# Kernel optimization log

Measured on AMD Instinct MI355X. Metric: run time of the kernel, lower is better.

The kernel has to match this reference:

```python
import jax, jax.numpy as jnp
import numpy as np

B = 1; H = 192; W = 192; DIM = 128; HEADS = 8
WS = 16                      # window_size
OWS = 24                     # overlap_win_size = int(16*0.5)+16
PAD = 4                      # (OWS-WS)//2
C2 = DIM // 2                # per-branch channels
H2 = HEADS // 2              # per-branch heads
HID = 256                    # mlp_ratio * dim
TBL = (WS + OWS - 1) ** 2    # 1521 rel-pos table entries
SCALE = (C2 // H2) ** (-0.5) # head_dim ** -0.5


def layer_norm(x, w, b, eps=1e-5):
    mu = jnp.mean(x, -1, keepdims=True)
    var = jnp.mean((x - mu) ** 2, -1, keepdims=True)
    return (x - mu) * jax.lax.rsqrt(var + eps) * w + b


def window_partition(x, ws):
    b, h, w, c = x.shape
    x = x.reshape(b, h // ws, ws, w // ws, ws, c).transpose(0, 1, 3, 2, 4, 5)
    return x.reshape(-1, ws, ws, c)


def window_reverse(win, ws, h, w):
    b = win.shape[0] // ((h // ws) * (w // ws))
    x = win.reshape(b, h // ws, w // ws, ws, ws, -1).transpose(0, 1, 3, 2, 4, 5)
    return x.reshape(b, h, w, -1)


def _patch_idx(h, w):
    ri = (jnp.arange(h // WS) * WS)[:, None] + jnp.arange(OWS)  # (nwh, OWS)
    ci = (jnp.arange(w // WS) * WS)[:, None] + jnp.arange(OWS)  # (nww, OWS)
    return ri, ci


def unfold_patches(x):
    # x: (b, h, w, c) -> (b*nw, OWS*OWS, c); matches nn.Unfold(OWS, stride=WS, pad=PAD)
    b, h, w, c = x.shape
    xp = jnp.pad(x, ((0, 0), (PAD, PAD), (PAD, PAD), (0, 0)))
    ri, ci = _patch_idx(h, w)
    p = xp[:, ri[:, None, :, None], ci[None, :, None, :], :]  # (b,nwh,nww,OWS,OWS,c)
    return p.reshape(-1, OWS * OWS, c)


def fold_patches(p, b, h, w):
    # inverse of unfold: scatter-add overlapping patches into (b, h+2PAD, w+2PAD, c)
    nwh, nww = h // WS, w // WS
    c = p.shape[-1]
    p = p.reshape(b, nwh, nww, OWS, OWS, c)
    ri, ci = _patch_idx(h, w)
    canvas = jnp.zeros((b, h + 2 * PAD, w + 2 * PAD, c), p.dtype)
    return canvas.at[:, ri[:, None, :, None], ci[None, :, None, :], :].add(p)


def cubic_kernel(x, A=-0.75):
    # PyTorch bicubic (cubic convolution, A=-0.75)
    ax = jnp.abs(x)
    w1 = ((A + 2.0) * ax - (A + 3.0)) * ax * ax + 1.0
    w2 = A * (ax * (ax * (ax - 5.0) + 8.0) - 4.0)
    return jnp.where(ax <= 1.0, w1, jnp.where(ax < 2.0, w2, 0.0))


def resize_matrix(n_out, n_in):
    # dense 1-D bicubic resize matrix, align_corners=False, border-clamped (torch semantics)
    i = jnp.arange(n_out, dtype=jnp.float32)
    src = (i + 0.5) * (float(n_in) / float(n_out)) - 0.5
    fl = jnp.floor(src)
    idx = fl[:, None] + jnp.arange(-1, 3, dtype=jnp.float32)[None, :]  # (n_out, 4)
    wts = cubic_kernel(src[:, None] - idx)
    idx_c = jnp.clip(idx, 0, n_in - 1).astype(jnp.int32)
    M = jnp.zeros((n_out, n_in), jnp.float32)
    return M.at[jnp.arange(n_out)[:, None], idx_c].add(wts)


def cross_attn(xq, xkv, rpi, wq, wkv, rpb):
    b_, nq, d = xq.shape
    n = xkv.shape[1]
    q = (xq @ wq).reshape(b_, nq, H2, -1).transpose(0, 2, 1, 3)
    k, v = jnp.split(xkv @ wkv, 2, axis=-1)
    k = k.reshape(b_, n, H2, -1).transpose(0, 2, 1, 3)
    v = v.reshape(b_, n, H2, -1).transpose(0, 2, 1, 3)
    attn = jnp.einsum('bhqd,bhkd->bhqk', q * SCALE, k)
    bias = rpb[rpi.reshape(-1)].reshape(WS * WS, OWS * OWS, H2)
    bias = bias.transpose(2, 0, 1) if nq < n else bias.transpose(2, 1, 0)
    attn = jax.nn.softmax(attn + bias[None], axis=-1)
    out = jnp.einsum('bhqk,bhkd->bhqd', attn, v)
    return out.transpose(0, 2, 1, 3).reshape(b_, nq, d)


def gsfn(x, h, w, fc1_w, fc1_b, sgn_w, sgn_b, conv_w, conv_b, fc2_w, fc2_b):
    x = x @ fc1_w + fc1_b  # NOTE: source GSFN never applies self.act
    x1, x2 = jnp.split(x, 2, axis=-1)
    Bn, N, Ch = x2.shape
    x2 = layer_norm(x2, sgn_w, sgn_b).transpose(0, 2, 1).reshape(Bn, Ch, h, w)
    x2 = jax.lax.conv_general_dilated(
        x2, conv_w, (1, 1), ((1, 1), (1, 1)),
        feature_group_count=Ch, dimension_numbers=('NCHW', 'OIHW', 'NCHW'))
    x2 = x2 + conv_b[None, :, None, None]
    x2 = x2.reshape(Bn, Ch, N).transpose(0, 2, 1)
    return (x1 * x2) @ fc2_w + fc2_b


def mstb(x_tkn, ln1_w, ln1_b, q1_w, kv1_w, rpb1, q2_w, kv2_w, rpb2,
         proj_w, proj_b, ln2_w, ln2_b, fc1_w, fc1_b, sgn_w, sgn_b,
         conv_w, conv_b, fc2_w, fc2_b, rpi, h, w):
    b, _, c = x_tkn.shape
    short = x_tkn
    x = layer_norm(x_tkn, ln1_w, ln1_b).reshape(b, h, w, c)
    xw = window_partition(x, WS).reshape(-1, WS * WS, c)     # (b*nw, ws*ws, c)
    xa, xb = jnp.split(xw, 2, axis=-1)
    xb_img = window_reverse(xb.reshape(-1, WS, WS, C2), WS, h, w)  # (b,h,w,C2)
    xb_p = unfold_patches(xb_img)                            # (b*nw, OWS*OWS, C2)
    a = cross_attn(xa, xb_p, rpi, q1_w, kv1_w, rpb1) + xa
    bb = cross_attn(xb_p, xa, rpi, q2_w, kv2_w, rpb2) + xb_p
    folded = fold_patches(bb, b, h, w)                       # (b, h+2p, w+2p, C2)
    Mh = resize_matrix(h, h + 2 * PAD)
    Mw = resize_matrix(w, w + 2 * PAD)
    resized = jnp.einsum('oi,bijc,pj->bopc', Mh, folded, Mw)  # bicubic to (h,w)
    xb2 = window_partition(resized, WS).reshape(-1, WS * WS, C2)
    x = jnp.concatenate([a, xb2], -1)
    x = window_reverse(x.reshape(-1, WS, WS, c), WS, h, w).reshape(b, h * w, c)
    x = x @ proj_w + proj_b + short
    x = gsfn(layer_norm(x, ln2_w, ln2_b), h, w, fc1_w, fc1_b,
             sgn_w, sgn_b, conv_w, conv_b, fc2_w, fc2_b) + x
    return x


def setup_inputs() -> dict:
    key = jax.random.key(0)
    ks = jax.random.split(key, 12)
    rn = lambda k, s, sc: jax.random.normal(k, s, jnp.float32) * sc
    return {
        'x_tkn': jax.random.normal(ks[0], (B, H * W, DIM), jnp.float32),
        'ln1_w': jnp.ones((DIM,), jnp.float32), 'ln1_b': jnp.zeros((DIM,), jnp.float32),
        'q1_w': rn(ks[1], (C2, C2), 0.05), 'kv1_w': rn(ks[2], (C2, 2 * C2), 0.05),
        'rpb1': rn(ks[3], (TBL, H2), 0.02),
        'q2_w': rn(ks[4], (C2, C2), 0.05), 'kv2_w': rn(ks[5], (C2, 2 * C2), 0.05),
        'rpb2': rn(ks[6], (TBL, H2), 0.02),
        'proj_w': rn(ks[7], (DIM, DIM), 0.05), 'proj_b': jnp.zeros((DIM,), jnp.float32),
        'ln2_w': jnp.ones((DIM,), jnp.float32), 'ln2_b': jnp.zeros((DIM,), jnp.float32),
        'fc1_w': rn(ks[8], (DIM, HID), 0.05), 'fc1_b': jnp.zeros((HID,), jnp.float32),
        'sgn_w': jnp.ones((HID // 2,), jnp.float32), 'sgn_b': jnp.zeros((HID // 2,), jnp.float32),
        'conv_w': rn(ks[9], (HID // 2, 1, 3, 3), 0.1), 'conv_b': jnp.zeros((HID // 2,), jnp.float32),
        'fc2_w': rn(ks[10], (HID // 2, DIM), 0.05), 'fc2_b': jnp.zeros((DIM,), jnp.float32),
        'rpi': jax.random.randint(ks[11], (WS * WS, OWS * OWS), 0, TBL),
        'h': H, 'w': W,
    }


def reference(x_tkn, ln1_w, ln1_b, q1_w, kv1_w, rpb1, q2_w, kv2_w, rpb2,
              proj_w, proj_b, ln2_w, ln2_b, fc1_w, fc1_b, sgn_w, sgn_b,
              conv_w, conv_b, fc2_w, fc2_b, rpi, h, w):
    return mstb(x_tkn, ln1_w, ln1_b, q1_w, kv1_w, rpb1, q2_w, kv2_w, rpb2,
                proj_w, proj_b, ln2_w, ln2_b, fc1_w, fc1_b, sgn_w, sgn_b,
                conv_w, conv_b, fc2_w, fc2_b, rpi, h, w)
```

## Files before the change

### kernel.cpp

```cpp
#include <hip/hip_runtime.h>
#include <hip/hip_bf16.h>

#define HH 192
#define WW 192
#define NWIN 12
#define WSZ 16
#define OWSZ 24
#define PADK 4
#define NQ1 256
#define NKV1 576
#define C2K 64
#define H2K 4
#define HD 16
#define NTOK (HH*WW)
#define LOG2E 1.4426950408889634f
#define QSCALE (0.25f * LOG2E)

typedef __hip_bfloat16 bf16;
typedef __attribute__((ext_vector_type(8))) short bf16x8;
typedef __attribute__((ext_vector_type(4))) float f32x4;

union B8 { short s[8]; bf16x8 v; unsigned u[4]; };

__device__ __forceinline__ unsigned cvtpk(float lo, float hi)
{
    unsigned r;
    asm("v_cvt_pk_bf16_f32 %0, %1, %2" : "=v"(r) : "v"(lo), "v"(hi));
    return r;
}

__launch_bounds__(256)
__global__ void ln_kernel(const float* __restrict__ in, int is, int io,
                          float* __restrict__ out, int os, int oo,
                          const float* __restrict__ g, const float* __restrict__ b,
                          int M)
{
    int row = blockIdx.x * 4 + (threadIdx.x >> 6);
    if (row >= M) return;
    int lane = threadIdx.x & 63;
    const float* p = in + (size_t)row * is + io;
    float v0 = p[lane * 2], v1 = p[lane * 2 + 1];
    float s = v0 + v1, sq = v0 * v0 + v1 * v1;
#pragma unroll
    for (int o = 32; o > 0; o >>= 1) { s += __shfl_xor(s, o); sq += __shfl_xor(sq, o); }
    float mu  = s * 0.0078125f;
    float var = fmaxf(sq * 0.0078125f - mu * mu, 0.f);
    float inv = 1.0f / sqrtf(var + 1e-5f);
    float* q = out + (size_t)row * os + oo;
    q[lane * 2]     = (v0 - mu) * inv * g[lane * 2]     + b[lane * 2];
    q[lane * 2 + 1] = (v1 - mu) * inv * g[lane * 2 + 1] + b[lane * 2 + 1];
}

__global__ void wcombT_kernel(const float* __restrict__ q1_w, const float* __restrict__ kv1_w,
                              const float* __restrict__ q2_w, const float* __restrict__ kv2_w,
                              bf16* __restrict__ WT)
{
    int idx = blockIdx.x * 256 + threadIdx.x;
    if (idx >= 384 * 128) return;
    int c = idx >> 7, r = idx & 127;
    float v = 0.f;
    if (c < 64)       { if (r < 64)  v = q1_w[r * 64 + c] * QSCALE; }
    else if (c < 192) { if (r >= 64) v = kv1_w[(r - 64) * 128 + (c - 64)]; }
    else if (c < 256) { if (r >= 64) v = q2_w[(r - 64) * 64 + (c - 192)] * QSCALE; }
    else              { if (r < 64)  v = kv2_w[r * 128 + (c - 256)]; }
    WT[idx] = __float2bfloat16(v);
}

__global__ void wtrans_kernel(const float* __restrict__ src, int N, bf16* __restrict__ dst)
{
    int idx = blockIdx.x * 256 + threadIdx.x;
    if (idx >= N * 128) return;
    int n = idx >> 7, k = idx & 127;
    dst[idx] = __float2bfloat16(src[(size_t)k * N + n]);
}

__global__ void bias1_kernel(const float* __restrict__ rpb1, const int* __restrict__ rpi,
                             float* __restrict__ biasT)
{
    int idx = blockIdx.x * 256 + threadIdx.x;
    if (idx >= H2K * NKV1 * NQ1) return;
    int q = idx & 255;
    int n = (idx >> 8) % NKV1;
    int h = idx / (NKV1 * NQ1);
    biasT[idx] = rpb1[rpi[q * NKV1 + n] * H2K + h] * LOG2E;
}

__global__ void bias2_kernel(const float* __restrict__ rpb2, const int* __restrict__ rpi,
                             float* __restrict__ biasT)
{
    int idx = blockIdx.x * 256 + threadIdx.x;
    if (idx >= H2K * NQ1 * NKV1) return;
    int q = idx % NKV1;
    int k = (idx / NKV1) % NQ1;
    int h = idx / (NKV1 * NQ1);
    biasT[idx] = rpb2[rpi[k * NKV1 + q] * H2K + h] * LOG2E;
}

template<int NTPW, bool OBF>
__launch_bounds__(256)
__global__ void gemm_mfma(const float* __restrict__ A1, int a1s,
                          const float* __restrict__ A2, int a2s,
                          const bf16* __restrict__ WT,
                          const float* __restrict__ bias,
                          const float* __restrict__ R, int rs,
                          float* __restrict__ C, int cs)
{
    const int tid = threadIdx.x;
    const int lane = tid & 63, w = tid >> 6;
    const int g = lane >> 4, nl = lane & 15;

    bf16x8 wf[NTPW][4];
#pragma unroll
    for (int t = 0; t < NTPW; t++) {
        const bf16* wp = WT + (size_t)((w * NTPW + t) * 16 + nl) * 128;
#pragma unroll
        for (int ks = 0; ks < 4; ks++)
            wf[t][ks] = *(const bf16x8*)(wp + ks * 32 + 8 * g);
    }

    const f32x4 zz = {0.f, 0.f, 0.f, 0.f};
    const int row = (blockIdx.x * 4 + blockIdx.y) * 16 + nl;

    bf16x8 xf[4];
    const float* ap = A1 + (size_t)row * a1s + 8 * g;
#pragma unroll
    for (int ks = 0; ks < 4; ks++) {
        float4 v0 = *(const float4*)(ap + ks * 32);
        float4 v1 = *(const float4*)(ap + ks * 32 + 4);
        if (A2) {
            const float* ap2 = A2 + (size_t)row * a2s + 8 * g + ks * 32;
            float4 m0 = *(const float4*)(ap2);
            float4 m1 = *(const float4*)(ap2 + 4);
            v0.x *= m0.x; v0.y *= m0.y; v0.z *= m0.z; v0.w *= m0.w;
            v1.x *= m1.x; v1.y *= m1.y; v1.z *= m1.z; v1.w *= m1.w;
        }
        B8 f;
        f.u[0] = cvtpk(v0.x, v0.y);
        f.u[1] = cvtpk(v0.z, v0.w);
        f.u[2] = cvtpk(v1.x, v1.y);
        f.u[3] = cvtpk(v1.z, v1.w);
        xf[ks] = f.v;
    }

    f32x4 acc[NTPW];
#pragma unroll
    for (int t = 0; t < NTPW; t++) acc[t] = zz;
#pragma unroll
    for (int ks = 0; ks < 4; ks++)
#pragma unroll
        for (int t = 0; t < NTPW; t++)
            acc[t] = __builtin_amdgcn_mfma_f32_16x16x32_bf16(wf[t][ks], xf[ks], acc[t], 0, 0, 0);

#pragma unroll
    for (int t = 0; t < NTPW; t++) {
        const int n0t = (w * NTPW + t) * 16 + 4 * g;
        if (OBF) {
            unsigned* Cu = (unsigned*)C + (size_t)row * (cs >> 1) + (n0t >> 1);
            uint2 o;
            o.x = cvtpk(acc[t][0], acc[t][1]);
            o.y = cvtpk(acc[t][2], acc[t][3]);
            *(uint2*)Cu = o;
        } else {
            float4 o;
            o.x = acc[t][0]; o.y = acc[t][1]; o.z = acc[t][2]; o.w = acc[t][3];
            if (bias) {
                float4 bv = *(const float4*)(bias + n0t);
                o.x += bv.x; o.y += bv.y; o.z += bv.z; o.w += bv.w;
            }
            if (R) {
                float4 rv = *(const float4*)(R + (size_t)row * rs + n0t);
                o.x += rv.x; o.y += rv.y; o.z += rv.z; o.w += rv.w;
            }
            *(float4*)(C + (size_t)row * cs + n0t) = o;
        }
    }
}

__launch_bounds__(256)
__global__ void attn1_mfma(const unsigned* __restrict__ qkvu,
                           const float* __restrict__ lnx,
                           const float* __restrict__ biasT,
                           float* __restrict__ xcat)
{
    __shared__ unsigned K_lds[NKV1][10];
    __shared__ unsigned V_lds[NKV1][10];

    const int win = blockIdx.x, h = blockIdx.y;
    const int wi = win / NWIN, wj = win % NWIN;
    const int tid = threadIdx.x;
    const int lane = tid & 63, w = tid >> 6;
    const int g = lane >> 4, qloc = lane & 15;

    for (int n = tid; n < NKV1; n += 256) {
        int rr = wi * WSZ - PADK + n / OWSZ, cc = wj * WSZ - PADK + n % OWSZ;
        bool ib = (rr >= 0 && rr < HH && cc >= 0 && cc < WW);
        uint4 k0v = make_uint4(0, 0, 0, 0), k1v = k0v, v0v = k0v, v1v = k0v;
        if (ib) {
            const unsigned* src = qkvu + (size_t)(rr * WW + cc) * 96 + 32 + 8 * h;
            k0v = *(const uint4*)(src);
            k1v = *(const uint4*)(src + 4);
            v0v = *(const uint4*)(src + 32);
            v1v = *(const uint4*)(src + 36);
        }
        *(uint4*)&K_lds[n][0] = k0v; *(uint4*)&K_lds[n][4] = k1v;
        *(uint4*)&V_lds[n][0] = v0v; *(uint4*)&V_lds[n][4] = v1v;
    }
    __syncthreads();

    const int q0base = blockIdx.z * 128 + w * 32;
    bf16x8 qfrag[2];
#pragma unroll
    for (int qt = 0; qt < 2; qt++) {
        int q = q0base + qt * 16 + qloc;
        int pix = (wi * WSZ + (q >> 4)) * WW + wj * WSZ + (q & 15);
        B8 f;
#pragma unroll
        for (int j = 0; j < 4; j++) f.u[j] = 0;
        if (g < 2)
            f.v = *(const bf16x8*)(qkvu + (size_t)pix * 96 + 8 * h + 4 * g);
        qfrag[qt] = f.v;
    }

    f32x4 O[2];
    float lsum[2];
#pragma unroll
    for (int qt = 0; qt < 2; qt++) { O[qt] = (f32x4){0.f, 0.f, 0.f, 0.f}; lsum[qt] = 0.f; }
    const f32x4 zz = {0.f, 0.f, 0.f, 0.f};

    for (int step = 0; step < 18; step++) {
        const int k0 = step * 32;
        bf16x8 kfA, kfB;
        if (g < 2) {
            kfA = *(const bf16x8*)&K_lds[k0 + qloc][4 * g];
            kfB = *(const bf16x8*)&K_lds[k0 + 16 + qloc][4 * g];
        } else {
            B8 zf;
#pragma unroll
            for (int j = 0; j < 4; j++) zf.u[j] = 0;
            kfA = zf.v; kfB = zf.v;
        }
        B8 vf;
#pragma unroll
        for (int j = 0; j < 8; j++) {
            int key = k0 + 4 * g + (j & 3) + ((j >> 2) << 4);
            unsigned word = V_lds[key][qloc >> 1];
            vf.s[j] = (short)((qloc & 1) ? (word >> 16) : (word & 0xffff));
        }

#pragma unroll
        for (int qt = 0; qt < 2; qt++) {
            f32x4 sA = __builtin_amdgcn_mfma_f32_16x16x32_bf16(kfA, qfrag[qt], zz, 0, 0, 0);
            f32x4 sB = __builtin_amdgcn_mfma_f32_16x16x32_bf16(kfB, qfrag[qt], zz, 0, 0, 0);
            int qa = q0base + qt * 16 + qloc;
            const float* bpA = biasT + ((size_t)h * NKV1 + k0 + 4 * g) * NQ1 + qa;
            const float* bpB = bpA + 16 * NQ1;
            float pa[4], pb[4];
            float ls = 0.f;
#pragma unroll
            for (int r = 0; r < 4; r++) {
                pa[r] = exp2f(sA[r] + bpA[(size_t)r * NQ1]);
                pb[r] = exp2f(sB[r] + bpB[(size_t)r * NQ1]);
                ls += pa[r] + pb[r];
            }
            B8 pf;
            pf.u[0] = cvtpk(pa[0], pa[1]);
            pf.u[1] = cvtpk(pa[2], pa[3]);
            pf.u[2] = cvtpk(pb[0], pb[1]);
            pf.u[3] = cvtpk(pb[2], pb[3]);
            lsum[qt] += ls;
            O[qt] = __builtin_amdgcn_mfma_f32_16x16x32_bf16(vf.v, pf.v, O[qt], 0, 0, 0);
        }
    }

#pragma unroll
    for (int qt = 0; qt < 2; qt++) {
        float lt = lsum[qt];
        lt += __shfl_xor(lt, 16);
        lt += __shfl_xor(lt, 32);
        float rl = 1.f / lt;
        int q = q0base + qt * 16 + qloc;
        int pix = (wi * WSZ + (q >> 4)) * WW + wj * WSZ + (q & 15);
        size_t base = (size_t)pix * 128 + h * HD + 4 * g;
#pragma unroll
        for (int r = 0; r < 4; r++)
            xcat[base + r] = O[qt][r] * rl + lnx[base + r];
    }
}

__launch_bounds__(256)
__global__ void attn2_mfma(const unsigned* __restrict__ qkvu,
                           const float* __restrict__ lnx,
                           const float* __restrict__ biasT,
                           float* __restrict__ bb)
{
    __shared__ unsigned K_lds[NQ1][10];
    __shared__ unsigned V_lds[NQ1][10];

    const int win = blockIdx.x, h = blockIdx.y;
    const int wi = win / NWIN, wj = win % NWIN;
    const int tid = threadIdx.x;
    const int lane = tid & 63, w = tid >> 6;
    const int g = lane >> 4, qloc = lane & 15;

    {
        int n = tid;
        int pix = (wi * WSZ + (n >> 4)) * WW + wj * WSZ + (n & 15);
        const unsigned* src = qkvu + (size_t)pix * 96 + 32 + 8 * h;
        *(uint4*)&K_lds[n][0] = *(const uint4*)(src);
        *(uint4*)&K_lds[n][4] = *(const uint4*)(src + 4);
        *(uint4*)&V_lds[n][0] = *(const uint4*)(src + 32);
        *(uint4*)&V_lds[n][4] = *(const uint4*)(src + 36);
    }
    __syncthreads();

    const int q0base = blockIdx.z * 192 + w * 48;
    bf16x8 qfrag[3];
    bool qin[3];
    int qpix[3];
#pragma unroll
    for (int qt = 0; qt < 3; qt++) {
        int qa = q0base + qt * 16 + qloc;
        int gr = wi * WSZ - PADK + qa / OWSZ, gc = wj * WSZ - PADK + qa % OWSZ;
        bool ib = (gr >= 0 && gr < HH && gc >= 0 && gc < WW);
        qin[qt] = ib;
        qpix[qt] = ib ? gr * WW + gc : 0;
        B8 f;
#pragma unroll
        for (int j = 0; j < 4; j++) f.u[j] = 0;
        if (ib && g < 2)
            f.v = *(const bf16x8*)(qkvu + (size_t)qpix[qt] * 96 + 8 * h + 4 * g);
        qfrag[qt] = f.v;
    }

    f32x4 O[3];
    float lsum[3];
#pragma unroll
    for (int qt = 0; qt < 3; qt++) { O[qt] = (f32x4){0.f, 0.f, 0.f, 0.f}; lsum[qt] = 0.f; }
    const f32x4 zz = {0.f, 0.f, 0.f, 0.f};

    for (int step = 0; step < 8; step++) {
        const int k0 = step * 32;
        bf16x8 kfA, kfB;
        if (g < 2) {
            kfA = *(const bf16x8*)&K_lds[k0 + qloc][4 * g];
            kfB = *(const bf16x8*)&K_lds[k0 + 16 + qloc][4 * g];
        } else {
            B8 zf;
#pragma unroll
            for (int j = 0; j < 4; j++) zf.u[j] = 0;
            kfA = zf.v; kfB = zf.v;
        }
        B8 vf;
#pragma unroll
        for (int j = 0; j < 8; j++) {
            int key = k0 + 4 * g + (j & 3) + ((j >> 2) << 4);
            unsigned word = V_lds[key][qloc >> 1];
            vf.s[j] = (short)((qloc & 1) ? (word >> 16) : (word & 0xffff));
        }

#pragma unroll
        for (int qt = 0; qt < 3; qt++) {
            f32x4 sA = __builtin_amdgcn_mfma_f32_16x16x32_bf16(kfA, qfrag[qt], zz, 0, 0, 0);
            f32x4 sB = __builtin_amdgcn_mfma_f32_16x16x32_bf16(kfB, qfrag[qt], zz, 0, 0, 0);
            int qa = q0base + qt * 16 + qloc;
            const float* bpA = biasT + ((size_t)h * NQ1 + k0 + 4 * g) * NKV1 + qa;
            const float* bpB = bpA + 16 * NKV1;
            float pa[4], pb[4];
            float ls = 0.f;
#pragma unroll
            for (int r = 0; r < 4; r++) {
                pa[r] = exp2f(sA[r] + bpA[(size_t)r * NKV1]);
                pb[r] = exp2f(sB[r] + bpB[(size_t)r * NKV1]);
                ls += pa[r] + pb[r];
            }
            B8 pf;
            pf.u[0] = cvtpk(pa[0], pa[1]);
            pf.u[1] = cvtpk(pa[2], pa[3]);
            pf.u[2] = cvtpk(pb[0], pb[1]);
            pf.u[3] = cvtpk(pb[2], pb[3]);
            lsum[qt] += ls;
            O[qt] = __builtin_amdgcn_mfma_f32_16x16x32_bf16(vf.v, pf.v, O[qt], 0, 0, 0);
        }
    }

#pragma unroll
    for (int qt = 0; qt < 3; qt++) {
        float lt = lsum[qt];
        lt += __shfl_xor(lt, 16);
        lt += __shfl_xor(lt, 32);
        float rl = 1.f / lt;
        int qa = q0base + qt * 16 + qloc;
        size_t obase = ((size_t)win * NKV1 + qa) * C2K + h * HD + 4 * g;
        size_t rbase = (size_t)qpix[qt] * 128 + C2K + h * HD + 4 * g;
#pragma unroll
        for (int r = 0; r < 4; r++)
            bb[obase + r] = O[qt][r] * rl + (qin[qt] ? lnx[rbase + r] : 0.f);
    }
}

__global__ void fold_kernel(const float* __restrict__ bb, float* __restrict__ folded)
{
    int idx = blockIdx.x * 256 + threadIdx.x;
    if (idx >= 200 * 200 * 64) return;
    int c = idx & 63;
    int j = (idx >> 6) % 200;
    int i = idx / (64 * 200);
    int ilo = (i > 23) ? ((i - 8) >> 4) : 0;
    int ihi = min(11, i >> 4);
    int jlo = (j > 23) ? ((j - 8) >> 4) : 0;
    int jhi = min(11, j >> 4);
    float s = 0.f;
    for (int wi = ilo; wi <= ihi; wi++)
        for (int wj = jlo; wj <= jhi; wj++) {
            int p = (i - wi * 16) * OWSZ + (j - wj * 16);
            s += bb[((size_t)(wi * NWIN + wj) * NKV1 + p) * C2K + c];
        }
    folded[idx] = s;
}

__device__ __forceinline__ float cubicw(float x)
{
    float ax = fabsf(x);
    const float A = -0.75f;
    if (ax <= 1.f) return ((A + 2.f) * ax - (A + 3.f)) * ax * ax + 1.f;
    if (ax < 2.f)  return A * (ax * (ax * (ax - 5.f) + 8.f) - 4.f);
    return 0.f;
}

__global__ void resize_kernel(const float* __restrict__ folded, float* __restrict__ xcat)
{
    int idx = blockIdx.x * 256 + threadIdx.x;
    if (idx >= HH * WW * C2K) return;
    int c = idx & 63;
    int p = (idx >> 6) % WW;
    int o = idx / (C2K * WW);
    const float ratio = 200.f / 192.f;
    float sr = (o + 0.5f) * ratio - 0.5f;
    float sc = (p + 0.5f) * ratio - 0.5f;
    int fr = (int)floorf(sr), fcc = (int)floorf(sc);
    float wc[4]; int ic[4];
#pragma unroll
    for (int u = 0; u < 4; u++) {
        int jj = fcc - 1 + u;
        wc[u] = cubicw(sc - (float)jj);
        ic[u] = min(max(jj, 0), 199);
    }
    float acc = 0.f;
#pragma unroll
    for (int t = 0; t < 4; t++) {
        int ii = fr - 1 + t;
        float wr = cubicw(sr - (float)ii);
        int ir = min(max(ii, 0), 199);
        const float* rowp = folded + ((size_t)ir * 200) * 64 + c;
        float rs = 0.f;
#pragma unroll
        for (int u = 0; u < 4; u++) rs += wc[u] * rowp[(size_t)ic[u] * 64];
        acc += wr * rs;
    }
    xcat[(size_t)(o * WW + p) * 128 + C2K + c] = acc;
}

__launch_bounds__(256)
__global__ void proj_ln2(const float* __restrict__ A1,
                         const bf16* __restrict__ WT,
                         const float* __restrict__ bias,
                         const float* __restrict__ R,
                         const float* __restrict__ ln2w, const float* __restrict__ ln2b,
                         float* __restrict__ xbuf, unsigned* __restrict__ ybf)
{
    __shared__ float psum[16][16];
    __shared__ float psq[16][16];
    __shared__ float mu_s[16], inv_s[16];

    const int tid = threadIdx.x;
    const int lane = tid & 63, w = tid >> 6;
    const int g = lane >> 4, nl = lane & 15;

    bf16x8 wf[2][4];
#pragma unroll
    for (int t = 0; t < 2; t++) {
        const bf16* wp = WT + (size_t)((w * 2 + t) * 16 + nl) * 128;
#pragma unroll
        for (int ks = 0; ks < 4; ks++)
            wf[t][ks] = *(const bf16x8*)(wp + ks * 32 + 8 * g);
    }

    const int row = (blockIdx.x * 4 + blockIdx.y) * 16 + nl;
    bf16x8 xf[4];
    const float* ap = A1 + (size_t)row * 128 + 8 * g;
#pragma unroll
    for (int ks = 0; ks < 4; ks++) {
        float4 v0 = *(const float4*)(ap + ks * 32);
        float4 v1 = *(const float4*)(ap + ks * 32 + 4);
        B8 f;
        f.u[0] = cvtpk(v0.x, v0.y);
        f.u[1] = cvtpk(v0.z, v0.w);
        f.u[2] = cvtpk(v1.x, v1.y);
        f.u[3] = cvtpk(v1.z, v1.w);
        xf[ks] = f.v;
    }

    const f32x4 zz = {0.f, 0.f, 0.f, 0.f};
    f32x4 acc[2];
    acc[0] = zz; acc[1] = zz;
#pragma unroll
    for (int ks = 0; ks < 4; ks++) {
        acc[0] = __builtin_amdgcn_mfma_f32_16x16x32_bf16(wf[0][ks], xf[ks], acc[0], 0, 0, 0);
        acc[1] = __builtin_amdgcn_mfma_f32_16x16x32_bf16(wf[1][ks], xf[ks], acc[1], 0, 0, 0);
    }

    float o[2][4];
    float s = 0.f, sq = 0.f;
#pragma unroll
    for (int t = 0; t < 2; t++) {
        int n0t = (w * 2 + t) * 16 + 4 * g;
        float4 bv = *(const float4*)(bias + n0t);
        float4 rv = *(const float4*)(R + (size_t)row * 128 + n0t);
        o[t][0] = acc[t][0] + bv.x + rv.x;
        o[t][1] = acc[t][1] + bv.y + rv.y;
        o[t][2] = acc[t][2] + bv.z + rv.z;
        o[t][3] = acc[t][3] + bv.w + rv.w;
#pragma unroll
        for (int r = 0; r < 4; r++) { s += o[t][r]; sq += o[t][r] * o[t][r]; }
    }
    psum[nl][w * 4 + g] = s;
    psq[nl][w * 4 + g] = sq;
    __syncthreads();
    if (tid < 16) {
        float ts = 0.f, tq = 0.f;
#pragma unroll
        for (int i = 0; i < 16; i++) { ts += psum[tid][i]; tq += psq[tid][i]; }
        float mu = ts * 0.0078125f;
        float var = fmaxf(tq * 0.0078125f - mu * mu, 0.f);
        mu_s[tid] = mu;
        inv_s[tid] = 1.0f / sqrtf(var + 1e-5f);
    }
    __syncthreads();

    float mu = mu_s[nl], inv = inv_s[nl];
#pragma unroll
    for (int t = 0; t < 2; t++) {
        int n0t = (w * 2 + t) * 16 + 4 * g;
        *(float4*)(xbuf + (size_t)row * 128 + n0t) = make_float4(o[t][0], o[t][1], o[t][2], o[t][3]);
        float4 gw = *(const float4*)(ln2w + n0t);
        float4 gb = *(const float4*)(ln2b + n0t);
        float y0 = (o[t][0] - mu) * inv * gw.x + gb.x;
        float y1 = (o[t][1] - mu) * inv * gw.y + gb.y;
        float y2 = (o[t][2] - mu) * inv * gw.z + gb.z;
        float y3 = (o[t][3] - mu) * inv * gw.w + gb.w;
        uint2 yo;
        yo.x = cvtpk(y0, y1);
        yo.y = cvtpk(y2, y3);
        *(uint2*)(ybf + (size_t)row * 64 + (n0t >> 1)) = yo;
    }
}

__launch_bounds__(256)
__global__ void fc1_sgn(const unsigned* __restrict__ ybf,
                        const bf16* __restrict__ WT,
                        const float* __restrict__ bias,
                        const float* __restrict__ sgnw, const float* __restrict__ sgnb,
                        float* __restrict__ h1)
{
    __shared__ float psum[16][8];
    __shared__ float psq[16][8];
    __shared__ float mu_s[16], inv_s[16];

    const int tid = threadIdx.x;
    const int lane = tid & 63, w = tid >> 6;
    const int g = lane >> 4, nl = lane & 15;

    bf16x8 wf[4][4];
#pragma unroll
    for (int t = 0; t < 4; t++) {
        const bf16* wp = WT + (size_t)((w * 4 + t) * 16 + nl) * 128;
#pragma unroll
        for (int ks = 0; ks < 4; ks++)
            wf[t][ks] = *(const bf16x8*)(wp + ks * 32 + 8 * g);
    }

    const int row = (blockIdx.x * 4 + blockIdx.y) * 16 + nl;
    bf16x8 xf[4];
    const unsigned* ap = ybf + (size_t)row * 64 + 4 * g;
#pragma unroll
    for (int ks = 0; ks < 4; ks++)
        xf[ks] = *(const bf16x8*)(ap + ks * 16);

    const f32x4 zz = {0.f, 0.f, 0.f, 0.f};
    f32x4 acc[4];
#pragma unroll
    for (int t = 0; t < 4; t++) acc[t] = zz;
#pragma unroll
    for (int ks = 0; ks < 4; ks++)
#pragma unroll
        for (int t = 0; t < 4; t++)
            acc[t] = __builtin_amdgcn_mfma_f32_16x16x32_bf16(wf[t][ks], xf[ks], acc[t], 0, 0, 0);

    float o[4][4];
    float s = 0.f, sq = 0.f;
#pragma unroll
    for (int t = 0; t < 4; t++) {
        int n0t = (w * 4 + t) * 16 + 4 * g;
        float4 bv = *(const float4*)(bias + n0t);
        o[t][0] = acc[t][0] + bv.x;
        o[t][1] = acc[t][1] + bv.y;
        o[t][2] = acc[t][2] + bv.z;
        o[t][3] = acc[t][3] + bv.w;
    }
    if (w >= 2) {
#pragma unroll
        for (int t = 0; t < 4; t++)
#pragma unroll
            for (int r = 0; r < 4; r++) { s += o[t][r]; sq += o[t][r] * o[t][r]; }
        psum[nl][(w - 2) * 4 + g] = s;
        psq[nl][(w - 2) * 4 + g] = sq;
    }
    __syncthreads();
    if (tid < 16) {
        float ts = 0.f, tq = 0.f;
#pragma unroll
        for (int i = 0; i < 8; i++) { ts += psum[tid][i]; tq += psq[tid][i]; }
        float mu = ts * 0.0078125f;
        float var = fmaxf(tq * 0.0078125f - mu * mu, 0.f);
        mu_s[tid] = mu;
        inv_s[tid] = 1.0f / sqrtf(var + 1e-5f);
    }
    __syncthreads();

    if (w < 2) {
#pragma unroll
        for (int t = 0; t < 4; t++) {
            int n0t = (w * 4 + t) * 16 + 4 * g;
            *(float4*)(h1 + (size_t)row * 256 + n0t) = make_float4(o[t][0], o[t][1], o[t][2], o[t][3]);
        }
    } else {
        float mu = mu_s[nl], inv = inv_s[nl];
#pragma unroll
        for (int t = 0; t < 4; t++) {
            int n0t = (w * 4 + t) * 16 + 4 * g;
            float4 gw = *(const float4*)(sgnw + n0t - 128);
            float4 gb = *(const float4*)(sgnb + n0t - 128);
            float4 y;
            y.x = (o[t][0] - mu) * inv * gw.x + gb.x;
            y.y = (o[t][1] - mu) * inv * gw.y + gb.y;
            y.z = (o[t][2] - mu) * inv * gw.z + gb.z;
            y.w = (o[t][3] - mu) * inv * gw.w + gb.w;
            *(float4*)(h1 + (size_t)row * 256 + n0t) = y;
        }
    }
}

__global__ void dwconv_kernel(const float* __restrict__ x2n,
                              const float* __restrict__ conv_w,
                              const float* __restrict__ conv_b,
                              float* __restrict__ x2c)
{
    int idx = blockIdx.x * 256 + threadIdx.x;
    if (idx >= NTOK * 128) return;
    int ch = idx & 127, t = idx >> 7;
    int i = t / WW, j = t % WW;
    float acc = conv_b[ch];
#pragma unroll
    for (int a = 0; a < 3; a++) {
        int ii = i + a - 1;
        if (ii < 0 || ii >= HH) continue;
#pragma unroll
        for (int b = 0; b < 3; b++) {
            int jj = j + b - 1;
            if (jj < 0 || jj >= WW) continue;
            acc += conv_w[ch * 9 + a * 3 + b] * x2n[(size_t)(ii * WW + jj) * 256 + ch];
        }
    }
    x2c[(size_t)t * 128 + ch] = acc;
}

extern "C" void kernel_launch(void* const* d_in, const int* in_sizes, int n_in,
                              void* d_out, int out_size, void* d_ws, size_t ws_size,
                              hipStream_t stream)
{
    (void)in_sizes; (void)n_in; (void)out_size; (void)ws_size;
    const float* x_tkn  = (const float*)d_in[0];
    const float* ln1_w  = (const float*)d_in[1];
    const float* ln1_b  = (const float*)d_in[2];
    const float* q1_w   = (const float*)d_in[3];
    const float* kv1_w  = (const float*)d_in[4];
    const float* rpb1   = (const float*)d_in[5];
    const float* q2_w   = (const float*)d_in[6];
    const float* kv2_w  = (const float*)d_in[7];
    const float* rpb2   = (const float*)d_in[8];
    const float* proj_w = (const float*)d_in[9];
    const float* proj_b = (const float*)d_in[10];
    const float* ln2_w  = (const float*)d_in[11];
    const float* ln2_b  = (const float*)d_in[12];
    const float* fc1_w  = (const float*)d_in[13];
    const float* fc1_b  = (const float*)d_in[14];
    const float* sgn_w  = (const float*)d_in[15];
    const float* sgn_b  = (const float*)d_in[16];
    const float* conv_w = (const float*)d_in[17];
    const float* conv_b = (const float*)d_in[18];
    const float* fc2_w  = (const float*)d_in[19];
    const float* fc2_b  = (const float*)d_in[20];
    const int*   rpi    = (const int*)d_in[21];

    float* ws = (float*)d_ws;
    float* lnx    = ws;
    float* xcat   = ws + 4718592;
    float* bbuf   = ws + 9437184;
    bf16*  projT  = (bf16*)(ws + 14155776);
    bf16*  fc1T   = (bf16*)(ws + 14163968);
    bf16*  fc2T   = (bf16*)(ws + 14180352);
    float* bias1T = ws + 14745600;
    float* bias2T = ws + 17104896;
    float* qkv    = ws + 17694720;
    bf16*  wcombT = (bf16*)(ws + 21233664);
    float* foldp  = ws + 17694720;
    float* h1     = ws + 14745600;
    float* out    = (float*)d_out;
    unsigned* ybf = (unsigned*)bbuf;

    ln_kernel<<<NTOK / 4, 256, 0, stream>>>(x_tkn, 128, 0, lnx, 128, 0, ln1_w, ln1_b, NTOK);
    wcombT_kernel<<<(384 * 128) / 256, 256, 0, stream>>>(q1_w, kv1_w, q2_w, kv2_w, wcombT);
    bias1_kernel<<<(H2K * NKV1 * NQ1) / 256, 256, 0, stream>>>(rpb1, rpi, bias1T);
    bias2_kernel<<<(H2K * NQ1 * NKV1) / 256, 256, 0, stream>>>(rpb2, rpi, bias2T);
    gemm_mfma<3, true><<<dim3(NTOK / 64, 4), 256, 0, stream>>>(lnx, 128, nullptr, 0, wcombT,
                                                               nullptr, nullptr, 0, qkv, 192);
    attn1_mfma<<<dim3(144, 4, 2), 256, 0, stream>>>((const unsigned*)qkv, lnx, bias1T, xcat);
    gemm_mfma<3, true><<<dim3(NTOK / 64, 4), 256, 0, stream>>>(lnx, 128, nullptr, 0,
                                                               wcombT + 192 * 128,
                                                               nullptr, nullptr, 0, qkv, 192);
    attn2_mfma<<<dim3(144, 4, 3), 256, 0, stream>>>((const unsigned*)qkv, lnx, bias2T, bbuf);
    fold_kernel<<<(200 * 200 * 64) / 256, 256, 0, stream>>>(bbuf, foldp);
    wtrans_kernel<<<(128 * 128) / 256, 256, 0, stream>>>(proj_w, 128, projT);
    wtrans_kernel<<<(256 * 128) / 256, 256, 0, stream>>>(fc1_w, 256, fc1T);
    wtrans_kernel<<<(128 * 128) / 256, 256, 0, stream>>>(fc2_w, 128, fc2T);
    resize_kernel<<<(HH * WW * C2K) / 256, 256, 0, stream>>>(foldp, xcat);
    proj_ln2<<<dim3(NTOK / 64, 4), 256, 0, stream>>>(xcat, projT, proj_b, x_tkn,
                                                     ln2_w, ln2_b, lnx, ybf);
    fc1_sgn<<<dim3(NTOK / 64, 4), 256, 0, stream>>>(ybf, fc1T, fc1_b, sgn_w, sgn_b, h1);
    dwconv_kernel<<<(NTOK * 128) / 256, 256, 0, stream>>>(h1 + 128, conv_w, conv_b, xcat);
    gemm_mfma<2, false><<<dim3(NTOK / 64, 4), 256, 0, stream>>>(h1, 256, xcat, 128, fc2T,
                                                                fc2_b, lnx, 128, out, 128);
}
```

Baseline: 305.1 us.

## Fuse LN1 into QKV GEMM, merge attention branches, bf16 MLP intermediates

LayerNorm1 is folded into a single QKV GEMM that computes all 384 output columns in one pass and also writes lnx. The two attention kernels become one launch that selects the branch from blockIdx, so both branches can run concurrently. The fc1/SGN outputs and the dwconv gating product are stored as bf16, with the gate multiply moved into dwconv, to cut memory traffic. The final GEMM then reads bf16 A directly, at some cost in intermediate precision.

After: 285.9 us. -6.3%, faster.

```diff
diff --git a/kernel.cpp b/kernel.cpp
--- a/kernel.cpp
+++ b/kernel.cpp
@@ -28,27 +28,9 @@
     asm("v_cvt_pk_bf16_f32 %0, %1, %2" : "=v"(r) : "v"(lo), "v"(hi));
     return r;
 }
-
-__launch_bounds__(256)
-__global__ void ln_kernel(const float* __restrict__ in, int is, int io,
-                          float* __restrict__ out, int os, int oo,
-                          const float* __restrict__ g, const float* __restrict__ b,
-                          int M)
-{
-    int row = blockIdx.x * 4 + (threadIdx.x >> 6);
-    if (row >= M) return;
-    int lane = threadIdx.x & 63;
-    const float* p = in + (size_t)row * is + io;
-    float v0 = p[lane * 2], v1 = p[lane * 2 + 1];
-    float s = v0 + v1, sq = v0 * v0 + v1 * v1;
-#pragma unroll
-    for (int o = 32; o > 0; o >>= 1) { s += __shfl_xor(s, o); sq += __shfl_xor(sq, o); }
-    float mu  = s * 0.0078125f;
-    float var = fmaxf(sq * 0.0078125f - mu * mu, 0.f);
-    float inv = 1.0f / sqrtf(var + 1e-5f);
-    float* q = out + (size_t)row * os + oo;
-    q[lane * 2]     = (v0 - mu) * inv * g[lane * 2]     + b[lane * 2];
-    q[lane * 2 + 1] = (v1 - mu) * inv * g[lane * 2 + 1] + b[lane * 2 + 1];
+__device__ __forceinline__ float bfu2f(unsigned short u)
+{
+    return __uint_as_float(((unsigned)u) << 16);
 }
 
 __global__ void wcombT_kernel(const float* __restrict__ q1_w, const float* __restrict__ kv1_w,
@@ -96,305 +78,307 @@
     biasT[idx] = rpb2[rpi[k * NKV1 + q] * H2K + h] * LOG2E;
 }
 
-template<int NTPW, bool OBF>
 __launch_bounds__(256)
-__global__ void gemm_mfma(const float* __restrict__ A1, int a1s,
-                          const float* __restrict__ A2, int a2s,
-                          const bf16* __restrict__ WT,
-                          const float* __restrict__ bias,
-                          const float* __restrict__ R, int rs,
-                          float* __restrict__ C, int cs)
+__global__ void gemm_qkv(const float* __restrict__ x_tkn,
+                         const float* __restrict__ ln1w, const float* __restrict__ ln1b,
+                         const bf16* __restrict__ WT,
+                         unsigned* __restrict__ qkvo, float* __restrict__ lnx)
 {
     const int tid = threadIdx.x;
     const int lane = tid & 63, w = tid >> 6;
     const int g = lane >> 4, nl = lane & 15;
 
-    bf16x8 wf[NTPW][4];
-#pragma unroll
-    for (int t = 0; t < NTPW; t++) {
-        const bf16* wp = WT + (size_t)((w * NTPW + t) * 16 + nl) * 128;
+    bf16x8 wf[6][4];
+#pragma unroll
+    for (int t = 0; t < 6; t++) {
+        const bf16* wp = WT + (size_t)((w * 6 + t) * 16 + nl) * 128;
 #pragma unroll
         for (int ks = 0; ks < 4; ks++)
             wf[t][ks] = *(const bf16x8*)(wp + ks * 32 + 8 * g);
     }
 
-    const f32x4 zz = {0.f, 0.f, 0.f, 0.f};
     const int row = (blockIdx.x * 4 + blockIdx.y) * 16 + nl;
-
-    bf16x8 xf[4];
-    const float* ap = A1 + (size_t)row * a1s + 8 * g;
+    const float* ap = x_tkn + (size_t)row * 128 + 8 * g;
+
+    float av[4][8];
+    float s = 0.f, sq = 0.f;
 #pragma unroll
     for (int ks = 0; ks < 4; ks++) {
         float4 v0 = *(const float4*)(ap + ks * 32);
         float4 v1 = *(const float4*)(ap + ks * 32 + 4);
-        if (A2) {
-            const float* ap2 = A2 + (size_t)row * a2s + 8 * g + ks * 32;
-            float4 m0 = *(const float4*)(ap2);
-            float4 m1 = *(const float4*)(ap2 + 4);
-            v0.x *= m0.x; v0.y *= m0.y; v0.z *= m0.z; v0.w *= m0.w;
-            v1.x *= m1.x; v1.y *= m1.y; v1.z *= m1.z; v1.w *= m1.w;
+        av[ks][0] = v0.x; av[ks][1] = v0.y; av[ks][2] = v0.z; av[ks][3] = v0.w;
+        av[ks][4] = v1.x; av[ks][5] = v1.y; av[ks][6] = v1.z; av[ks][7] = v1.w;
+#pragma unroll
+        for (int j = 0; j < 8; j++) { s += av[ks][j]; sq += av[ks][j] * av[ks][j]; }
+    }
+    s  += __shfl_xor(s, 16);  s  += __shfl_xor(s, 32);
+    sq += __shfl_xor(sq, 16); sq += __shfl_xor(sq, 32);
+    float mu  = s * 0.0078125f;
+    float var = fmaxf(sq * 0.0078125f - mu * mu, 0.f);
+    float inv = 1.0f / sqrtf(var + 1e-5f);
+
+    bf16x8 xf[4];
+#pragma unroll
+    for (int ks = 0; ks < 4; ks++) {
+        int col = ks * 32 + 8 * g;
+        float4 g0 = *(const float4*)(ln1w + col);
+        float4 g1 = *(const float4*)(ln1w + col + 4);
+        float4 b0 = *(const float4*)(ln1b + col);
+        float4 b1 = *(const float4*)(ln1b + col + 4);
+        float nv[8];
+        nv[0] = (av[ks][0] - mu) * inv * g0.x + b0.x;
+        nv[1] = (av[ks][1] - mu) * inv * g0.y + b0.y;
+        nv[2] = (av[ks][2] - mu) * inv * g0.z + b0.z;
+        nv[3] = (av[ks][3] - mu) * inv * g0.w + b0.w;
+        nv[4] = (av[ks][4] - mu) * inv * g1.x + b1.x;
+        nv[5] = (av[ks][5] - mu) * inv * g1.y + b1.y;
+        nv[6] = (av[ks][6] - mu) * inv * g1.z + b1.z;
+        nv[7] = (av[ks][7] - mu) * inv * g1.w + b1.w;
+        if (w == 0) {
+            float* lp = lnx + (size_t)row * 128 + col;
+            *(float4*)lp       = make_float4(nv[0], nv[1], nv[2], nv[3]);
+            *(float4*)(lp + 4) = make_float4(nv[4], nv[5], nv[6], nv[7]);
         }
         B8 f;
-        f.u[0] = cvtpk(v0.x, v0.y);
-        f.u[1] = cvtpk(v0.z, v0.w);
-        f.u[2] = cvtpk(v1.x, v1.y);
-        f.u[3] = cvtpk(v1.z, v1.w);
+        f.u[0] = cvtpk(nv[0], nv[1]);
+        f.u[1] = cvtpk(nv[2], nv[3]);
+        f.u[2] = cvtpk(nv[4], nv[5]);
+        f.u[3] = cvtpk(nv[6], nv[7]);
         xf[ks] = f.v;
     }
 
-    f32x4 acc[NTPW];
-#pragma unroll
-    for (int t = 0; t < NTPW; t++) acc[t] = zz;
+    const f32x4 zz = {0.f, 0.f, 0.f, 0.f};
+    f32x4 acc[6];
+#pragma unroll
+    for (int t = 0; t < 6; t++) acc[t] = zz;
 #pragma unroll
     for (int ks = 0; ks < 4; ks++)
 #pragma unroll
-        for (int t = 0; t < NTPW; t++)
+        for (int t = 0; t < 6; t++)
             acc[t] = __builtin_amdgcn_mfma_f32_16x16x32_bf16(wf[t][ks], xf[ks], acc[t], 0, 0, 0);
 
 #pragma unroll
-    for (int t = 0; t < NTPW; t++) {
-        const int n0t = (w * NTPW + t) * 16 + 4 * g;
-        if (OBF) {
-            unsigned* Cu = (unsigned*)C + (size_t)row * (cs >> 1) + (n0t >> 1);
-            uint2 o;
-            o.x = cvtpk(acc[t][0], acc[t][1]);
-            o.y = cvtpk(acc[t][2], acc[t][3]);
-            *(uint2*)Cu = o;
-        } else {
-            float4 o;
-            o.x = acc[t][0]; o.y = acc[t][1]; o.z = acc[t][2]; o.w = acc[t][3];
-            if (bias) {
-                float4 bv = *(const float4*)(bias + n0t);
-                o.x += bv.x; o.y += bv.y; o.z += bv.z; o.w += bv.w;
-            }
-            if (R) {
-                float4 rv = *(const float4*)(R + (size_t)row * rs + n0t);
-                o.x += rv.x; o.y += rv.y; o.z += rv.z; o.w += rv.w;
-            }
-            *(float4*)(C + (size_t)row * cs + n0t) = o;
-        }
+    for (int t = 0; t < 6; t++) {
+        int n0t = (w * 6 + t) * 16 + 4 * g;
+        uint2 o;
+        o.x = cvtpk(acc[t][0], acc[t][1]);
+        o.y = cvtpk(acc[t][2], acc[t][3]);
+        *(uint2*)(qkvo + (size_t)row * 192 + (n0t >> 1)) = o;
     }
 }
 
 __launch_bounds__(256)
-__global__ void attn1_mfma(const unsigned* __restrict__ qkvu,
+__global__ void attn_fused(const unsigned* __restrict__ qkvu,
                            const float* __restrict__ lnx,
-                           const float* __restrict__ biasT,
-                           float* __restrict__ xcat)
+                           const float* __restrict__ bias1T,
+                           const float* __restrict__ bias2T,
+                           float* __restrict__ xcat,
+                           float* __restrict__ bb)
 {
     __shared__ unsigned K_lds[NKV1][10];
     __shared__ unsigned V_lds[NKV1][10];
 
-    const int win = blockIdx.x, h = blockIdx.y;
-    const int wi = win / NWIN, wj = win % NWIN;
+    const int h = blockIdx.y;
     const int tid = threadIdx.x;
     const int lane = tid & 63, w = tid >> 6;
     const int g = lane >> 4, qloc = lane & 15;
-
-    for (int n = tid; n < NKV1; n += 256) {
-        int rr = wi * WSZ - PADK + n / OWSZ, cc = wj * WSZ - PADK + n % OWSZ;
-        bool ib = (rr >= 0 && rr < HH && cc >= 0 && cc < WW);
-        uint4 k0v = make_uint4(0, 0, 0, 0), k1v = k0v, v0v = k0v, v1v = k0v;
-        if (ib) {
-            const unsigned* src = qkvu + (size_t)(rr * WW + cc) * 96 + 32 + 8 * h;
-            k0v = *(const uint4*)(src);
-            k1v = *(const uint4*)(src + 4);
-            v0v = *(const uint4*)(src + 32);
-            v1v = *(const uint4*)(src + 36);
-        }
-        *(uint4*)&K_lds[n][0] = k0v; *(uint4*)&K_lds[n][4] = k1v;
-        *(uint4*)&V_lds[n][0] = v0v; *(uint4*)&V_lds[n][4] = v1v;
-    }
-    __syncthreads();
-
-    const int q0base = blockIdx.z * 128 + w * 32;
-    bf16x8 qfrag[2];
-#pragma unroll
-    for (int qt = 0; qt < 2; qt++) {
-        int q = q0base + qt * 16 + qloc;
-        int pix = (wi * WSZ + (q >> 4)) * WW + wj * WSZ + (q & 15);
-        B8 f;
-#pragma unroll
-        for (int j = 0; j < 4; j++) f.u[j] = 0;
-        if (g < 2)
-            f.v = *(const bf16x8*)(qkvu + (size_t)pix * 96 + 8 * h + 4 * g);
-        qfrag[qt] = f.v;
-    }
-
-    f32x4 O[2];
-    float lsum[2];
-#pragma unroll
-    for (int qt = 0; qt < 2; qt++) { O[qt] = (f32x4){0.f, 0.f, 0.f, 0.f}; lsum[qt] = 0.f; }
     const f32x4 zz = {0.f, 0.f, 0.f, 0.f};
 
-    for (int step = 0; step < 18; step++) {
-        const int k0 = step * 32;
-        bf16x8 kfA, kfB;
-        if (g < 2) {
-            kfA = *(const bf16x8*)&K_lds[k0 + qloc][4 * g];
-            kfB = *(const bf16x8*)&K_lds[k0 + 16 + qloc][4 * g];
-        } else {
-            B8 zf;
-#pragma unroll
-            for (int j = 0; j < 4; j++) zf.u[j] = 0;
-            kfA = zf.v; kfB = zf.v;
-        }
-        B8 vf;
-#pragma unroll
-        for (int j = 0; j < 8; j++) {
-            int key = k0 + 4 * g + (j & 3) + ((j >> 2) << 4);
-            unsigned word = V_lds[key][qloc >> 1];
-            vf.s[j] = (short)((qloc & 1) ? (word >> 16) : (word & 0xffff));
-        }
-
+    if (blockIdx.x < 288) {
+        const int win = blockIdx.x % 144, z = blockIdx.x / 144;
+        const int wi = win / NWIN, wj = win % NWIN;
+
+        for (int n = tid; n < NKV1; n += 256) {
+            int rr = wi * WSZ - PADK + n / OWSZ, cc = wj * WSZ - PADK + n % OWSZ;
+            bool ib = (rr >= 0 && rr < HH && cc >= 0 && cc < WW);
+            uint4 k0v = make_uint4(0, 0, 0, 0), k1v = k0v, v0v = k0v, v1v = k0v;
+            if (ib) {
+                const unsigned* src = qkvu + (size_t)(rr * WW + cc) * 192 + 32 + 8 * h;
+                k0v = *(const uint4*)(src);
+                k1v = *(const uint4*)(src + 4);
+                v0v = *(const uint4*)(src + 32);
+                v1v = *(const uint4*)(src + 36);
+            }
+            *(uint4*)&K_lds[n][0] = k0v; *(uint4*)&K_lds[n][4] = k1v;
+            *(uint4*)&V_lds[n][0] = v0v; *(uint4*)&V_lds[n][4] = v1v;
+        }
+        __syncthreads();
+
+        const int q0base = z * 128 + w * 32;
+        bf16x8 qfrag[2];
 #pragma unroll
         for (int qt = 0; qt < 2; qt++) {
-            f32x4 sA = __builtin_amdgcn_mfma_f32_16x16x32_bf16(kfA, qfrag[qt], zz, 0, 0, 0);
-            f32x4 sB = __builtin_amdgcn_mfma_f32_16x16x32_bf16(kfB, qfrag[qt], zz, 0, 0, 0);
+            int q = q0base + qt * 16 + qloc;
+            int pix = (wi * WSZ + (q >> 4)) * WW + wj * WSZ + (q & 15);
+            B8 f;
+#pragma unroll
+            for (int j = 0; j < 4; j++) f.u[j] = 0;
+            if (g < 2)
+                f.v = *(const bf16x8*)(qkvu + (size_t)pix * 192 + 8 * h + 4 * g);
+            qfrag[qt] = f.v;
+        }
+
+        f32x4 O[2];
+        float lsum[2];
+#pragma unroll
+        for (int qt = 0; qt < 2; qt++) { O[qt] = zz; lsum[qt] = 0.f; }
+
+        for (int step = 0; step < 18; step++) {
+            const int k0 = step * 32;
+            bf16x8 kfA, kfB;
+            if (g < 2) {
+                kfA = *(const bf16x8*)&K_lds[k0 + qloc][4 * g];
+                kfB = *(const bf16x8*)&K_lds[k0 + 16 + qloc][4 * g];
+            } else {
+                B8 zf;
+#pragma unroll
+                for (int j = 0; j < 4; j++) zf.u[j] = 0;
+                kfA = zf.v; kfB = zf.v;
+            }
+            B8 vf;
+#pragma unroll
+            for (int j = 0; j < 8; j++) {
+                int key = k0 + 4 * g + (j & 3) + ((j >> 2) << 4);
+                unsigned word = V_lds[key][qloc >> 1];
+                vf.s[j] = (short)((qloc & 1) ? (word >> 16) : (word & 0xffff));
+            }
+
+#pragma unroll
+            for (int qt = 0; qt < 2; qt++) {
+                f32x4 sA = __builtin_amdgcn_mfma_f32_16x16x32_bf16(kfA, qfrag[qt], zz, 0, 0, 0);
+                f32x4 sB = __builtin_amdgcn_mfma_f32_16x16x32_bf16(kfB, qfrag[qt], zz, 0, 0, 0);
+                int qa = q0base + qt * 16 + qloc;
+                const float* bpA = bias1T + ((size_t)h * NKV1 + k0 + 4 * g) * NQ1 + qa;
+                const float* bpB = bpA + 16 * NQ1;
+                float pa[4], pb[4];
+                float ls = 0.f;
+#pragma unroll
+                for (int r = 0; r < 4; r++) {
+                    pa[r] = exp2f(sA[r] + bpA[(size_t)r * NQ1]);
+                    pb[r] = exp2f(sB[r] + bpB[(size_t)r * NQ1]);
+                    ls += pa[r] + pb[r];
+                }
+                B8 pf;
+                pf.u[0] = cvtpk(pa[0], pa[1]);
+                pf.u[1] = cvtpk(pa[2], pa[3]);
+                pf.u[2] = cvtpk(pb[0], pb[1]);
+                pf.u[3] = cvtpk(pb[2], pb[3]);
+                lsum[qt] += ls;
+                O[qt] = __builtin_amdgcn_mfma_f32_16x16x32_bf16(vf.v, pf.v, O[qt], 0, 0, 0);
+            }
+        }
+
+#pragma unroll
+        for (int qt = 0; qt < 2; qt++) {
+            float lt = lsum[qt];
+            lt += __shfl_xor(lt, 16);
+            lt += __shfl_xor(lt, 32);
+            float rl = 1.f / lt;
+            int q = q0base + qt * 16 + qloc;
+            int pix = (wi * WSZ + (q >> 4)) * WW + wj * WSZ + (q & 15);
+            size_t base = (size_t)pix * 128 + h * HD + 4 * g;
+#pragma unroll
+            for (int r = 0; r < 4; r++)
+                xcat[base + r] = O[qt][r] * rl + lnx[base + r];
+        }
+    } else {
+        const int bx = blockIdx.x - 288;
+        const int win = bx % 144, z = bx / 144;
+        const int wi = win / NWIN, wj = win % NWIN;
+
+        {
+            int n = tid;
+            int pix = (wi * WSZ + (n >> 4)) * WW + wj * WSZ + (n & 15);
+            const unsigned* src = qkvu + (size_t)pix * 192 + 128 + 8 * h;
+            *(uint4*)&K_lds[n][0] = *(const uint4*)(src);
+            *(uint4*)&K_lds[n][4] = *(const uint4*)(src + 4);
+            *(uint4*)&V_lds[n][0] = *(const uint4*)(src + 32);
+            *(uint4*)&V_lds[n][4] = *(const uint4*)(src + 36);
+        }
+        __syncthreads();
+
+        const int q0base = z * 192 + w * 48;
+        bf16x8 qfrag[3];
+        bool qin[3];
+        int qpix[3];
+#pragma unroll
+        for (int qt = 0; qt < 3; qt++) {
             int qa = q0base + qt * 16 + qloc;
-            const float* bpA = biasT + ((size_t)h * NKV1 + k0 + 4 * g) * NQ1 + qa;
-            const float* bpB = bpA + 16 * NQ1;
-            float pa[4], pb[4];
-            float ls = 0.f;
-#pragma unroll
-            for (int r = 0; r < 4; r++) {
-                pa[r] = exp2f(sA[r] + bpA[(size_t)r * NQ1]);
-                pb[r] = exp2f(sB[r] + bpB[(size_t)r * NQ1]);
-                ls += pa[r] + pb[r];
+            int gr = wi * WSZ - PADK + qa / OWSZ, gc = wj * WSZ - PADK + qa % OWSZ;
+            bool ib = (gr >= 0 && gr < HH && gc >= 0 && gc < WW);
+            qin[qt] = ib;
+            qpix[qt] = ib ? gr * WW + gc : 0;
+            B8 f;
+#pragma unroll
+            for (int j = 0; j < 4; j++) f.u[j] = 0;
+            if (ib && g < 2)
+                f.v = *(const bf16x8*)(qkvu + (size_t)qpix[qt] * 192 + 96 + 8 * h + 4 * g);
+            qfrag[qt] = f.v;
+        }
+
+        f32x4 O[3];
+        float lsum[3];
+#pragma unroll
+        for (int qt = 0; qt < 3; qt++) { O[qt] = zz; lsum[qt] = 0.f; }
+
+        for (int step = 0; step < 8; step++) {
+            const int k0 = step * 32;
+            bf16x8 kfA, kfB;
+            if (g < 2) {
+                kfA = *(const bf16x8*)&K_lds[k0 + qloc][4 * g];
+                kfB = *(const bf16x8*)&K_lds[k0 + 16 + qloc][4 * g];
+            } else {
+                B8 zf;
+#pragma unroll
+                for (int j = 0; j < 4; j++) zf.u[j] = 0;
+                kfA = zf.v; kfB = zf.v;
             }
-            B8 pf;
-            pf.u[0] = cvtpk(pa[0], pa[1]);
-            pf.u[1] = cvtpk(pa[2], pa[3]);
-            pf.u[2] = cvtpk(pb[0], pb[1]);
-            pf.u[3] = cvtpk(pb[2], pb[3]);
-            lsum[qt] += ls;
-            O[qt] = __builtin_amdgcn_mfma_f32_16x16x32_bf16(vf.v, pf.v, O[qt], 0, 0, 0);
-        }
-    }
-
-#pragma unroll
-    for (int qt = 0; qt < 2; qt++) {
-        float lt = lsum[qt];
-        lt += __shfl_xor(lt, 16);
-        lt += __shfl_xor(lt, 32);
-        float rl = 1.f / lt;
-        int q = q0base + qt * 16 + qloc;
-        int pix = (wi * WSZ + (q >> 4)) * WW + wj * WSZ + (q & 15);
-        size_t base = (size_t)pix * 128 + h * HD + 4 * g;
-#pragma unroll
-        for (int r = 0; r < 4; r++)
-            xcat[base + r] = O[qt][r] * rl + lnx[base + r];
-    }
-}
-
-__launch_bounds__(256)
-__global__ void attn2_mfma(const unsigned* __restrict__ qkvu,
-                           const float* __restrict__ lnx,
-                           const float* __restrict__ biasT,
-                           float* __restrict__ bb)
-{
-    __shared__ unsigned K_lds[NQ1][10];
-    __shared__ unsigned V_lds[NQ1][10];
-
-    const int win = blockIdx.x, h = blockIdx.y;
-    const int wi = win / NWIN, wj = win % NWIN;
-    const int tid = threadIdx.x;
-    const int lane = tid & 63, w = tid >> 6;
-    const int g = lane >> 4, qloc = lane & 15;
-
-    {
-        int n = tid;
-        int pix = (wi * WSZ + (n >> 4)) * WW + wj * WSZ + (n & 15);
-        const unsigned* src = qkvu + (size_t)pix * 96 + 32 + 8 * h;
-        *(uint4*)&K_lds[n][0] = *(const uint4*)(src);
-        *(uint4*)&K_lds[n][4] = *(const uint4*)(src + 4);
-        *(uint4*)&V_lds[n][0] = *(const uint4*)(src + 32);
-        *(uint4*)&V_lds[n][4] = *(const uint4*)(src + 36);
-    }
-    __syncthreads();
-
-    const int q0base = blockIdx.z * 192 + w * 48;
-    bf16x8 qfrag[3];
-    bool qin[3];
-    int qpix[3];
-#pragma unroll
-    for (int qt = 0; qt < 3; qt++) {
-        int qa = q0base + qt * 16 + qloc;
-        int gr = wi * WSZ - PADK + qa / OWSZ, gc = wj * WSZ - PADK + qa % OWSZ;
-        bool ib = (gr >= 0 && gr < HH && gc >= 0 && gc < WW);
-        qin[qt] = ib;
-        qpix[qt] = ib ? gr * WW + gc : 0;
-        B8 f;
-#pragma unroll
-        for (int j = 0; j < 4; j++) f.u[j] = 0;
-        if (ib && g < 2)
-            f.v = *(const bf16x8*)(qkvu + (size_t)qpix[qt] * 96 + 8 * h + 4 * g);
-        qfrag[qt] = f.v;
-    }
-
-    f32x4 O[3];
-    float lsum[3];
-#pragma unroll
-    for (int qt = 0; qt < 3; qt++) { O[qt] = (f32x4){0.f, 0.f, 0.f, 0.f}; lsum[qt] = 0.f; }
-    const f32x4 zz = {0.f, 0.f, 0.f, 0.f};
-
-    for (int step = 0; step < 8; step++) {
-        const int k0 = step * 32;
-        bf16x8 kfA, kfB;
-        if (g < 2) {
-            kfA = *(const bf16x8*)&K_lds[k0 + qloc][4 * g];
-            kfB = *(const bf16x8*)&K_lds[k0 + 16 + qloc][4 * g];
-        } else {
-            B8 zf;
-#pragma unroll
-            for (int j = 0; j < 4; j++) zf.u[j] = 0;
-            kfA = zf.v; kfB = zf.v;
-        }
-        B8 vf;
-#pragma unroll
-        for (int j = 0; j < 8; j++) {
-            int key = k0 + 4 * g + (j & 3) + ((j >> 2) << 4);
-            unsigned word = V_lds[key][qloc >> 1];
-            vf.s[j] = (short)((qloc & 1) ? (word >> 16) : (word & 0xffff));
+            B8 vf;
+#pragma unroll
+            for (int j = 0; j < 8; j++) {
+                int key = k0 + 4 * g + (j & 3) + ((j >> 2) << 4);
+                unsigned word = V_lds[key][qloc >> 1];
+                vf.s[j] = (short)((qloc & 1) ? (word >> 16) : (word & 0xffff));
+            }
+
+#pragma unroll
+            for (int qt = 0; qt < 3; qt++) {
+                f32x4 sA = __builtin_amdgcn_mfma_f32_16x16x32_bf16(kfA, qfrag[qt], zz, 0, 0, 0);
+                f32x4 sB = __builtin_amdgcn_mfma_f32_16x16x32_bf16(kfB, qfrag[qt], zz, 0, 0, 0);
+                int qa = q0base + qt * 16 + qloc;
+                const float* bpA = bias2T + ((size_t)h * NQ1 + k0 + 4 * g) * NKV1 + qa;
+                const float* bpB = bpA + 16 * NKV1;
+                float pa[4], pb[4];
+                float ls = 0.f;
+#pragma unroll
+                for (int r = 0; r < 4; r++) {
+                    pa[r] = exp2f(sA[r] + bpA[(size_t)r * NKV1]);
+                    pb[r] = exp2f(sB[r] + bpB[(size_t)r * NKV1]);
+                    ls += pa[r] + pb[r];
+                }
+                B8 pf;
+                pf.u[0] = cvtpk(pa[0], pa[1]);
+                pf.u[1] = cvtpk(pa[2], pa[3]);
+                pf.u[2] = cvtpk(pb[0], pb[1]);
+                pf.u[3] = cvtpk(pb[2], pb[3]);
+                lsum[qt] += ls;
+                O[qt] = __builtin_amdgcn_mfma_f32_16x16x32_bf16(vf.v, pf.v, O[qt], 0, 0, 0);
+            }
         }
 
 #pragma unroll
         for (int qt = 0; qt < 3; qt++) {
-            f32x4 sA = __builtin_amdgcn_mfma_f32_16x16x32_bf16(kfA, qfrag[qt], zz, 0, 0, 0);
-            f32x4 sB = __builtin_amdgcn_mfma_f32_16x16x32_bf16(kfB, qfrag[qt], zz, 0, 0, 0);
+            float lt = lsum[qt];
+            lt += __shfl_xor(lt, 16);
+            lt += __shfl_xor(lt, 32);
+            float rl = 1.f / lt;
             int qa = q0base + qt * 16 + qloc;
-            const float* bpA = biasT + ((size_t)h * NQ1 + k0 + 4 * g) * NKV1 + qa;
-            const float* bpB = bpA + 16 * NKV1;
-            float pa[4], pb[4];
-            float ls = 0.f;
-#pragma unroll
-            for (int r = 0; r < 4; r++) {
-                pa[r] = exp2f(sA[r] + bpA[(size_t)r * NKV1]);
-                pb[r] = exp2f(sB[r] + bpB[(size_t)r * NKV1]);
-                ls += pa[r] + pb[r];
-            }
-            B8 pf;
-            pf.u[0] = cvtpk(pa[0], pa[1]);
-            pf.u[1] = cvtpk(pa[2], pa[3]);
-            pf.u[2] = cvtpk(pb[0], pb[1]);
-            pf.u[3] = cvtpk(pb[2], pb[3]);
-            lsum[qt] += ls;
-            O[qt] = __builtin_amdgcn_mfma_f32_16x16x32_bf16(vf.v, pf.v, O[qt], 0, 0, 0);
-        }
-    }
-
-#pragma unroll
-    for (int qt = 0; qt < 3; qt++) {
-        float lt = lsum[qt];
-        lt += __shfl_xor(lt, 16);
-        lt += __shfl_xor(lt, 32);
-        float rl = 1.f / lt;
-        int qa = q0base + qt * 16 + qloc;
-        size_t obase = ((size_t)win * NKV1 + qa) * C2K + h * HD + 4 * g;
-        size_t rbase = (size_t)qpix[qt] * 128 + C2K + h * HD + 4 * g;
-#pragma unroll
-        for (int r = 0; r < 4; r++)
-            bb[obase + r] = O[qt][r] * rl + (qin[qt] ? lnx[rbase + r] : 0.f);
+            size_t obase = ((size_t)win * NKV1 + qa) * C2K + h * HD + 4 * g;
+            size_t rbase = (size_t)qpix[qt] * 128 + C2K + h * HD + 4 * g;
+#pragma unroll
+            for (int r = 0; r < 4; r++)
+                bb[obase + r] = O[qt][r] * rl + (qin[qt] ? lnx[rbase + r] : 0.f);
+        }
     }
 }
 
@@ -560,7 +544,7 @@
                         const bf16* __restrict__ WT,
                         const float* __restrict__ bias,
                         const float* __restrict__ sgnw, const float* __restrict__ sgnb,
-                        float* __restrict__ h1)
+                        unsigned* __restrict__ x1b, unsigned* __restrict__ x2b)
 {
     __shared__ float psum[16][8];
     __shared__ float psq[16][8];
@@ -631,29 +615,36 @@
 #pragma unroll
         for (int t = 0; t < 4; t++) {
             int n0t = (w * 4 + t) * 16 + 4 * g;
-            *(float4*)(h1 + (size_t)row * 256 + n0t) = make_float4(o[t][0], o[t][1], o[t][2], o[t][3]);
+            uint2 xo;
+            xo.x = cvtpk(o[t][0], o[t][1]);
+            xo.y = cvtpk(o[t][2], o[t][3]);
+            *(uint2*)(x1b + (size_t)row * 64 + (n0t >> 1)) = xo;
         }
     } else {
         float mu = mu_s[nl], inv = inv_s[nl];
 #pragma unroll
         for (int t = 0; t < 4; t++) {
             int n0t = (w * 4 + t) * 16 + 4 * g;
-            float4 gw = *(const float4*)(sgnw + n0t - 128);
-            float4 gb = *(const float4*)(sgnb + n0t - 128);
-            float4 y;
-            y.x = (o[t][0] - mu) * inv * gw.x + gb.x;
-            y.y = (o[t][1] - mu) * inv * gw.y + gb.y;
-            y.z = (o[t][2] - mu) * inv * gw.z + gb.z;
-            y.w = (o[t][3] - mu) * inv * gw.w + gb.w;
-            *(float4*)(h1 + (size_t)row * 256 + n0t) = y;
-        }
-    }
-}
-
-__global__ void dwconv_kernel(const float* __restrict__ x2n,
+            int m0t = n0t - 128;
+            float4 gw = *(const float4*)(sgnw + m0t);
+            float4 gb = *(const float4*)(sgnb + m0t);
+            float y0 = (o[t][0] - mu) * inv * gw.x + gb.x;
+            float y1 = (o[t][1] - mu) * inv * gw.y + gb.y;
+            float y2 = (o[t][2] - mu) * inv * gw.z + gb.z;
+            float y3 = (o[t][3] - mu) * inv * gw.w + gb.w;
+            uint2 xo;
+            xo.x = cvtpk(y0, y1);
+            xo.y = cvtpk(y2, y3);
+            *(uint2*)(x2b + (size_t)row * 64 + (m0t >> 1)) = xo;
+        }
+    }
+}
+
+__global__ void dwconv_kernel(const unsigned short* __restrict__ x2b,
+                              const unsigned short* __restrict__ x1b,
                               const float* __restrict__ conv_w,
                               const float* __restrict__ conv_b,
-                              float* __restrict__ x2c)
+                              unsigned short* __restrict__ ab)
 {
     int idx = blockIdx.x * 256 + threadIdx.x;
     if (idx >= NTOK * 128) return;
@@ -668,10 +659,62 @@
         for (int b = 0; b < 3; b++) {
             int jj = j + b - 1;
             if (jj < 0 || jj >= WW) continue;
-            acc += conv_w[ch * 9 + a * 3 + b] * x2n[(size_t)(ii * WW + jj) * 256 + ch];
-        }
-    }
-    x2c[(size_t)t * 128 + ch] = acc;
+            acc += conv_w[ch * 9 + a * 3 + b] * bfu2f(x2b[(size_t)(ii * WW + jj) * 128 + ch]);
+        }
+    }
+    float prod = bfu2f(x1b[(size_t)t * 128 + ch]) * acc;
+    unsigned u = __float_as_uint(prod);
+    ab[(size_t)t * 128 + ch] = (unsigned short)((u + 0x7FFFu + ((u >> 16) & 1u)) >> 16);
+}
+
+__launch_bounds__(256)
+__global__ void gemm_bfA(const unsigned* __restrict__ Au,
+                         const bf16* __restrict__ WT,
+                         const float* __restrict__ bias,
+                         const float* __restrict__ R,
+                         float* __restrict__ C)
+{
+    const int tid = threadIdx.x;
+    const int lane = tid & 63, w = tid >> 6;
+    const int g = lane >> 4, nl = lane & 15;
+
+    bf16x8 wf[2][4];
+#pragma unroll
+    for (int t = 0; t < 2; t++) {
+        const bf16* wp = WT + (size_t)((w * 2 + t) * 16 + nl) * 128;
+#pragma unroll
+        for (int ks = 0; ks < 4; ks++)
+            wf[t][ks] = *(const bf16x8*)(wp + ks * 32 + 8 * g);
+    }
+
+    const int row = (blockIdx.x * 4 + blockIdx.y) * 16 + nl;
+    bf16x8 xf[4];
+    const unsigned* ap = Au + (size_t)row * 64 + 4 * g;
+#pragma unroll
+    for (int ks = 0; ks < 4; ks++)
+        xf[ks] = *(const bf16x8*)(ap + ks * 16);
+
+    const f32x4 zz = {0.f, 0.f, 0.f, 0.f};
+    f32x4 acc[2];
+    acc[0] = zz; acc[1] = zz;
+#pragma unroll
+    for (int ks = 0; ks < 4; ks++) {
+        acc[0] = __builtin_amdgcn_mfma_f32_16x16x32_bf16(wf[0][ks], xf[ks], acc[0], 0, 0, 0);
+        acc[1] = __builtin_amdgcn_mfma_f32_16x16x32_bf16(wf[1][ks], xf[ks], acc[1], 0, 0, 0);
+    }
+
+#pragma unroll
+    for (int t = 0; t < 2; t++) {
+        const int n0t = (w * 2 + t) * 16 + 4 * g;
+        float4 bv = *(const float4*)(bias + n0t);
+        float4 rv = *(const float4*)(R + (size_t)row * 128 + n0t);
+        float4 o;
+        o.x = acc[t][0] + bv.x + rv.x;
+        o.y = acc[t][1] + bv.y + rv.y;
+        o.z = acc[t][2] + bv.z + rv.z;
+        o.w = acc[t][3] + bv.w + rv.w;
+        *(float4*)(C + (size_t)row * 128 + n0t) = o;
+    }
 }
 
 extern "C" void kernel_launch(void* const* d_in, const int* in_sizes, int n_in,
@@ -712,23 +755,21 @@
     float* bias1T = ws + 14745600;
     float* bias2T = ws + 17104896;
     float* qkv    = ws + 17694720;
-    bf16*  wcombT = (bf16*)(ws + 21233664);
+    bf16*  wcombT = (bf16*)(ws + 24772608);
     float* foldp  = ws + 17694720;
-    float* h1     = ws + 14745600;
+    unsigned* ybf = (unsigned*)bbuf;
+    unsigned* x1b = (unsigned*)(ws + 14745600);
+    unsigned* x2b = (unsigned*)(ws + 17104896);
+    unsigned* ab  = (unsigned*)(ws + 19464192);
     float* out    = (float*)d_out;
-    unsigned* ybf = (unsigned*)bbuf;
-
-    ln_kernel<<<NTOK / 4, 256, 0, stream>>>(x_tkn, 128, 0, lnx, 128, 0, ln1_w, ln1_b, NTOK);
+
     wcombT_kernel<<<(384 * 128) / 256, 256, 0, stream>>>(q1_w, kv1_w, q2_w, kv2_w, wcombT);
     bias1_kernel<<<(H2K * NKV1 * NQ1) / 256, 256, 0, stream>>>(rpb1, rpi, bias1T);
     bias2_kernel<<<(H2K * NQ1 * NKV1) / 256, 256, 0, stream>>>(rpb2, rpi, bias2T);
-    gemm_mfma<3, true><<<dim3(NTOK / 64, 4), 256, 0, stream>>>(lnx, 128, nullptr, 0, wcombT,
-                                                               nullptr, nullptr, 0, qkv, 192);
-    attn1_mfma<<<dim3(144, 4, 2), 256, 0, stream>>>((const unsigned*)qkv, lnx, bias1T, xcat);
-    gemm_mfma<3, true><<<dim3(NTOK / 64, 4), 256, 0, stream>>>(lnx, 128, nullptr, 0,
-                                                               wcombT + 192 * 128,
-                                                               nullptr, nullptr, 0, qkv, 192);
-    attn2_mfma<<<dim3(144, 4, 3), 256, 0, stream>>>((const unsigned*)qkv, lnx, bias2T, bbuf);
+    gemm_qkv<<<dim3(NTOK / 64, 4), 256, 0, stream>>>(x_tkn, ln1_w, ln1_b, wcombT,
+                                                     (unsigned*)qkv, lnx);
+    attn_fused<<<dim3(720, 4), 256, 0, stream>>>((const unsigned*)qkv, lnx,
+                                                 bias1T, bias2T, xcat, bbuf);
     fold_kernel<<<(200 * 200 * 64) / 256, 256, 0, stream>>>(bbuf, foldp);
     wtrans_kernel<<<(128 * 128) / 256, 256, 0, stream>>>(proj_w, 128, projT);
     wtrans_kernel<<<(256 * 128) / 256, 256, 0, stream>>>(fc1_w, 256, fc1T);
@@ -736,8 +777,10 @@
     resize_kernel<<<(HH * WW * C2K) / 256, 256, 0, stream>>>(foldp, xcat);
     proj_ln2<<<dim3(NTOK / 64, 4), 256, 0, stream>>>(xcat, projT, proj_b, x_tkn,
                                                      ln2_w, ln2_b, lnx, ybf);
-    fc1_sgn<<<dim3(NTOK / 64, 4), 256, 0, stream>>>(ybf, fc1T, fc1_b, sgn_w, sgn_b, h1);
-    dwconv_kernel<<<(NTOK * 128) / 256, 256, 0, stream>>>(h1 + 128, conv_w, conv_b, xcat);
-    gemm_mfma<2, false><<<dim3(NTOK / 64, 4), 256, 0, stream>>>(h1, 256, xcat, 128, fc2T,
-                                                                fc2_b, lnx, 128, out, 128);
-}
+    fc1_sgn<<<dim3(NTOK / 64, 4), 256, 0, stream>>>(ybf, fc1T, fc1_b, sgn_w, sgn_b, x1b, x2b);
+    dwconv_kernel<<<(NTOK * 128) / 256, 256, 0, stream>>>((const unsigned short*)x2b,
+                                                          (const unsigned short*)x1b,
+                                                          conv_w, conv_b,
+                                                          (unsigned short*)ab);
+    gemm_bfA<<<dim3(NTOK / 64, 4), 256, 0, stream>>>(ab, fc2T, fc2_b, lnx, out);
+}
```
